# Performance work log

Hardware: AMD Instinct MI355X
Metric: run time of the kernel (lower is better)

The kernel has to match this reference:

```python
import jax, jax.numpy as jnp
import numpy as np

N = 50000      # nodes
E = 1_600_000  # edges (avg degree 32)
G = 2000       # graphs in batch
H = 2          # attention heads
C = 64         # out_channels
IN = 64        # in_channels
NEG_SLOPE = 0.2


def setup_inputs() -> dict:
    key = jax.random.key(0)
    ks = jax.random.split(key, 6)
    x = jax.random.normal(ks[0], (N, IN), dtype=jnp.float32)
    edge_index = jax.random.randint(ks[1], (2, E), 0, N, dtype=jnp.int32)
    batch = jnp.sort(jax.random.randint(ks[2], (N,), 0, G, dtype=jnp.int32))
    # GATConv params: lin weight [H*C, IN] (glorot-ish), att vectors, bias [C]
    W = jax.random.normal(ks[3], (H * C, IN), dtype=jnp.float32) * (1.0 / np.sqrt(IN))
    att_src = jax.random.normal(ks[4], (1, H, C), dtype=jnp.float32) * 0.1
    att_dst = jax.random.normal(ks[5], (1, H, C), dtype=jnp.float32) * 0.1
    bias = jnp.zeros((C,), dtype=jnp.float32)
    return {"x": x, "edge_index": edge_index, "batch": batch,
            "W": W, "att_src": att_src, "att_dst": att_dst, "bias": bias}


def reference(x, edge_index, batch, W, att_src, att_dst, bias):
    # --- GATConv (PyG semantics: add_self_loops=True, concat=False -> head mean + bias) ---
    loops = jnp.arange(N, dtype=edge_index.dtype)
    src = jnp.concatenate([edge_index[0], loops])  # [E+N]
    dst = jnp.concatenate([edge_index[1], loops])  # [E+N]

    xp = (x @ W.T).reshape(N, H, C)                 # projected node feats [N,H,C]
    a_src = jnp.sum(xp * att_src, axis=-1)          # [N,H]
    a_dst = jnp.sum(xp * att_dst, axis=-1)          # [N,H]

    e = jax.nn.leaky_relu(a_src[src] + a_dst[dst], NEG_SLOPE)  # [E+N,H]
    # segment softmax over incoming edges of each destination node
    m = jax.ops.segment_max(e, dst, num_segments=N)            # [N,H]
    e = jnp.exp(e - m[dst])
    s = jax.ops.segment_sum(e, dst, num_segments=N)            # [N,H]
    alpha = e / s[dst]                                         # [E+N,H]

    msg = xp[src] * alpha[:, :, None]                          # [E+N,H,C]
    out = jax.ops.segment_sum(msg, dst, num_segments=N)        # [N,H,C]
    h_nodes = out.mean(axis=1) + bias                          # [N,C]

    # --- global_mean_pool ---
    sums = jax.ops.segment_sum(h_nodes, batch, num_segments=G)                     # [G,C]
    cnt = jax.ops.segment_sum(jnp.ones((N, 1), h_nodes.dtype), batch, num_segments=G)
    h_graphs = sums / jnp.maximum(cnt, 1.0)                                        # [G,C]
    return (h_nodes, h_graphs)
```

## Files before the change

### kernel.cpp

```cpp
#include <hip/hip_runtime.h>
#include <hip/hip_bf16.h>

#define H 2
#define C 64
#define IN_CH 64
#define HC (H*C)
#define NEG_SLOPE 0.2f
#define NBUCK_MAX 256
#define NBLK 1024

__global__ __launch_bounds__(128) void proj_kernel(
    const float* __restrict__ x, const float* __restrict__ W,
    const float* __restrict__ att_src, const float* __restrict__ att_dst,
    __hip_bfloat16* __restrict__ xp, float* __restrict__ asrc,
    float* __restrict__ adst, int N) {
    int t = threadIdx.x;
    float w[64];
    const float4* wr = reinterpret_cast<const float4*>(W + (size_t)t * IN_CH);
#pragma unroll
    for (int q = 0; q < 16; q++) {
        float4 v = wr[q];
        w[4 * q] = v.x; w[4 * q + 1] = v.y; w[4 * q + 2] = v.z; w[4 * q + 3] = v.w;
    }
    float a_s = att_src[t], a_d = att_dst[t];
    int lane = t & 63, head = t >> 6;
    for (int n = blockIdx.x; n < N; n += gridDim.x) {
        const float* xr = x + (size_t)n * IN_CH;
        float acc = 0.f;
#pragma unroll
        for (int k = 0; k < 64; k++) acc = fmaf(w[k], xr[k], acc);
        xp[(size_t)n * HC + t] = __float2bfloat16(acc);
        float as = acc * a_s, ad = acc * a_d;
#pragma unroll
        for (int d = 32; d > 0; d >>= 1) {
            as += __shfl_xor(as, d, 64);
            ad += __shfl_xor(ad, d, 64);
        }
        if (lane == 0) {
            asrc[(size_t)n * H + head] = as;
            adst[(size_t)n * H + head] = ad;
        }
    }
}

__global__ __launch_bounds__(256) void hist_kernel(const int* __restrict__ dstE,
                                                   int* __restrict__ hist,
                                                   int E, int nbuck, int chunkE) {
    __shared__ int lh[NBUCK_MAX];
    for (int t = threadIdx.x; t < nbuck; t += 256) lh[t] = 0;
    __syncthreads();
    int beg = blockIdx.x * chunkE;
    int end = min(beg + chunkE, E);
    for (int i = beg + threadIdx.x; i < end; i += 256)
        atomicAdd(&lh[dstE[i] >> 8], 1);
    __syncthreads();
    for (int t = threadIdx.x; t < nbuck; t += 256)
        hist[t * NBLK + blockIdx.x] = lh[t];
}

__global__ __launch_bounds__(256) void scan_rows_kernel(int* __restrict__ hist,
                                                        int* __restrict__ rowsum) {
    int b = blockIdx.x, t = threadIdx.x;
    int* row = hist + b * NBLK;
    int v[4];
    int s = 0;
#pragma unroll
    for (int j = 0; j < 4; j++) { v[j] = row[t * 4 + j]; s += v[j]; }
    __shared__ int sh[256];
    sh[t] = s;
    __syncthreads();
    for (int d = 1; d < 256; d <<= 1) {
        int u = (t >= d) ? sh[t - d] : 0;
        __syncthreads();
        sh[t] += u;
        __syncthreads();
    }
    int run = sh[t] - s;
#pragma unroll
    for (int j = 0; j < 4; j++) { row[t * 4 + j] = run; run += v[j]; }
    if (t == 255) rowsum[b] = sh[255];
}

__global__ __launch_bounds__(256) void scan_base_kernel(int* __restrict__ rowsum,
                                                        int* __restrict__ bucketBase,
                                                        int nbuck) {
    int t = threadIdx.x;
    int v = (t < nbuck) ? rowsum[t] : 0;
    __shared__ int sh[256];
    sh[t] = v;
    __syncthreads();
    for (int d = 1; d < 256; d <<= 1) {
        int u = (t >= d) ? sh[t - d] : 0;
        __syncthreads();
        sh[t] += u;
        __syncthreads();
    }
    if (t < nbuck) bucketBase[t] = sh[t] - v;
    if (t == nbuck - 1) bucketBase[nbuck] = sh[t];
}

__global__ __launch_bounds__(256) void bucket_scatter_kernel(
    const int* __restrict__ srcE, const int* __restrict__ dstE,
    const int* __restrict__ hist, const int* __restrict__ bucketBase,
    int* __restrict__ staged, int E, int nbuck, int chunkE) {
    __shared__ int cur[NBUCK_MAX];
    for (int t = threadIdx.x; t < nbuck; t += 256)
        cur[t] = hist[t * NBLK + blockIdx.x] + bucketBase[t];
    __syncthreads();
    int beg = blockIdx.x * chunkE;
    int end = min(beg + chunkE, E);
    for (int i = beg + threadIdx.x; i < end; i += 256) {
        int s = srcE[i], d = dstE[i];
        int pos = atomicAdd(&cur[d >> 8], 1);
        staged[pos] = s | ((d & 255) << 20);
    }
}

__global__ __launch_bounds__(512) void bucket_csr_kernel(
    const int* __restrict__ staged, const int* __restrict__ bucketBase,
    int* __restrict__ off, int* __restrict__ csr, int N) {
    int b = blockIdx.x, t = threadIdx.x;
    int beg = bucketBase[b], end = bucketBase[b + 1];
    __shared__ int lh[256], sh[256], cur[256];
    if (t < 256) lh[t] = 0;
    __syncthreads();
    for (int i = beg + t; i < end; i += 512)
        atomicAdd(&lh[staged[i] >> 20], 1);
    __syncthreads();
    int v = (t < 256) ? lh[t] : 0;
    if (t < 256) sh[t] = v;
    __syncthreads();
    for (int d = 1; d < 256; d <<= 1) {
        int u = (t >= d && t < 256) ? sh[t - d] : 0;
        __syncthreads();
        if (t < 256) sh[t] += u;
        __syncthreads();
    }
    if (t < 256) {
        int ex = sh[t] - v;
        int nd = b * 256 + t;
        if (nd < N) off[nd] = beg + ex;
        if (nd == N - 1) off[N] = end;
        cur[t] = beg + ex;
    }
    __syncthreads();
    for (int i = beg + t; i < end; i += 512) {
        int e = staged[i];
        int pos = atomicAdd(&cur[e >> 20], 1);
        csr[pos] = e & 0xFFFFF;
    }
}

__global__ __launch_bounds__(256) void aggregate_kernel(
    const __hip_bfloat16* __restrict__ xp, const float2* __restrict__ asrc,
    const float2* __restrict__ adst, const int* __restrict__ off,
    const int* __restrict__ csr, const float* __restrict__ bias,
    const int* __restrict__ batch, float* __restrict__ out,
    float* __restrict__ gsum, int* __restrict__ gcnt, int N) {
    __shared__ float4 stage[4][64];
    int wid = threadIdx.x >> 6;
    int n = blockIdx.x * 4 + wid;
    if (n >= N) return;
    int lane = threadIdx.x & 63;
    float4* st = stage[wid];
    int o0 = off[n];
    int degE = off[n + 1] - o0;
    float2 ad = adst[n];
    float2 asn = asrc[n];
    float es0 = asn.x + ad.x; es0 = (es0 > 0.f) ? es0 : NEG_SLOPE * es0;
    float es1 = asn.y + ad.y; es1 = (es1 > 0.f) ? es1 : NEG_SLOPE * es1;
    float ws0 = __expf(es0), ws1 = __expf(es1);
    float s0 = (lane == 0) ? ws0 : 0.f;
    float s1 = (lane == 0) ? ws1 : 0.f;

    const uint* xpw = reinterpret_cast<const uint*>(xp);
    float accx, accy;
    {
        float wgt = (lane < 32) ? ws0 : ws1;
        uint u = xpw[(size_t)n * 64 + lane];
        accx = wgt * __uint_as_float(u << 16);
        accy = wgt * __uint_as_float(u & 0xffff0000u);
    }

    for (int base = 0; base < degE; base += 64) {
        int i = base + lane;
        int idx = 0;
        float w0 = 0.f, w1 = 0.f;
        if (i < degE) {
            idx = csr[o0 + i];
            float2 as = asrc[idx];
            float t0 = as.x + ad.x; t0 = (t0 > 0.f) ? t0 : NEG_SLOPE * t0;
            float t1 = as.y + ad.y; t1 = (t1 > 0.f) ? t1 : NEG_SLOPE * t1;
            w0 = __expf(t0);
            w1 = __expf(t1);
        }
        s0 += w0;
        s1 += w1;
        st[lane] = make_float4(__int_as_float(idx), w0, w1, 0.f);
        int cnt = min(degE - base, 64);
        int nb16 = (cnt + 15) >> 4;
        for (int b = 0; b < nb16; b++) {
            float4 e[16];
#pragma unroll
            for (int j = 0; j < 16; j++) e[j] = st[b * 16 + j];
            uint bu[16];
#pragma unroll
            for (int j = 0; j < 16; j++) {
                int s2 = __float_as_int(e[j].x);
                bu[j] = xpw[(size_t)s2 * 64 + lane];
            }
#pragma unroll
            for (int j = 0; j < 16; j++) {
                float wgt = (lane < 32) ? e[j].y : e[j].z;
                accx = fmaf(wgt, __uint_as_float(bu[j] << 16), accx);
                accy = fmaf(wgt, __uint_as_float(bu[j] & 0xffff0000u), accy);
            }
        }
    }
#pragma unroll
    for (int d = 32; d > 0; d >>= 1) {
        s0 += __shfl_xor(s0, d, 64);
        s1 += __shfl_xor(s1, d, 64);
    }
    float inv = (lane < 32) ? (1.f / s0) : (1.f / s1);
    accx *= inv;
    accy *= inv;
    float ox = 0.5f * (accx + __shfl_xor(accx, 32, 64));
    float oy = 0.5f * (accy + __shfl_xor(accy, 32, 64));
    int g = batch[n];
    if (lane < 32) {
        float vx = ox + bias[2 * lane];
        float vy = oy + bias[2 * lane + 1];
        *reinterpret_cast<float2*>(out + (size_t)n * C + 2 * lane) = make_float2(vx, vy);
        atomicAdd(&gsum[(size_t)g * C + 2 * lane], vx);
        atomicAdd(&gsum[(size_t)g * C + 2 * lane + 1], vy);
    }
    if (lane == 0) atomicAdd(&gcnt[g], 1);
}

__global__ void pool_kernel(const float* __restrict__ gsum, const int* __restrict__ gcnt,
                            float* __restrict__ out, int G, int baseOff) {
    int i = blockIdx.x * blockDim.x + threadIdx.x;
    if (i >= G * C) return;
    int g = i >> 6;
    float cnt = (float)max(gcnt[g], 1);
    out[baseOff + i] = gsum[i] / cnt;
}

extern "C" void kernel_launch(void* const* d_in, const int* in_sizes, int n_in,
                              void* d_out, int out_size, void* d_ws, size_t ws_size,
                              hipStream_t stream) {
    const float* x       = (const float*)d_in[0];
    const int*   edge    = (const int*)d_in[1];
    const int*   batch   = (const int*)d_in[2];
    const float* W       = (const float*)d_in[3];
    const float* att_src = (const float*)d_in[4];
    const float* att_dst = (const float*)d_in[5];
    const float* bias    = (const float*)d_in[6];

    int N = in_sizes[0] / IN_CH;
    int E = in_sizes[1] / 2;
    int G = out_size / C - N;
    int nbuck = (N + 255) >> 8;
    int chunkE = (E + NBLK - 1) / NBLK;

    char* p = (char*)d_ws;
    auto alloc = [&](size_t bytes) {
        char* r = p;
        p += (bytes + 255) & ~(size_t)255;
        return r;
    };
    __hip_bfloat16* xp = (__hip_bfloat16*)alloc((size_t)N * HC * 2);
    float* asrc    = (float*)alloc((size_t)N * H * 4);
    float* adst    = (float*)alloc((size_t)N * H * 4);
    int*   hist    = (int*)alloc((size_t)nbuck * NBLK * 4);
    int*   rowsum  = (int*)alloc((size_t)(nbuck + 1) * 4);
    int*   bucketBase = (int*)alloc((size_t)(nbuck + 1) * 4);
    int*   off     = (int*)alloc((size_t)(N + 1) * 4);
    int*   staged  = (int*)alloc((size_t)E * 4);
    int*   csr     = (int*)alloc((size_t)E * 4);
    float* gsum    = (float*)alloc((size_t)G * C * 4);
    int*   gcnt    = (int*)alloc((size_t)G * 4);

    hipMemsetAsync(gsum, 0, (size_t)G * C * 4, stream);
    hipMemsetAsync(gcnt, 0, (size_t)G * 4, stream);

    const int* srcE = edge;
    const int* dstE = edge + E;

    proj_kernel<<<2048, 128, 0, stream>>>(x, W, att_src, att_dst, xp, asrc, adst, N);
    hist_kernel<<<NBLK, 256, 0, stream>>>(dstE, hist, E, nbuck, chunkE);
    scan_rows_kernel<<<nbuck, 256, 0, stream>>>(hist, rowsum);
    scan_base_kernel<<<1, 256, 0, stream>>>(rowsum, bucketBase, nbuck);
    bucket_scatter_kernel<<<NBLK, 256, 0, stream>>>(srcE, dstE, hist, bucketBase,
                                                    staged, E, nbuck, chunkE);
    bucket_csr_kernel<<<nbuck, 512, 0, stream>>>(staged, bucketBase, off, csr, N);
    aggregate_kernel<<<(N + 3) / 4, 256, 0, stream>>>(xp, (const float2*)asrc, (const float2*)adst,
                                                      off, csr, bias, batch,
                                                      (float*)d_out, gsum, gcnt, N);
    pool_kernel<<<(G * C + 255) / 256, 256, 0, stream>>>(gsum, gcnt, (float*)d_out, G, N * C);
}
```

Measured before the change: 235.7 us.

## Fuse base scan into scatter/CSR kernels, split LDS staging, replace atomic pooling

```diff
diff --git a/kernel.cpp b/kernel.cpp
--- a/kernel.cpp
+++ b/kernel.cpp
@@ -81,35 +81,34 @@
     if (t == 255) rowsum[b] = sh[255];
 }
 
-__global__ __launch_bounds__(256) void scan_base_kernel(int* __restrict__ rowsum,
-                                                        int* __restrict__ bucketBase,
-                                                        int nbuck) {
-    int t = threadIdx.x;
+__device__ __forceinline__ void base_scan(const int* rowsum, int nbuck,
+                                          int* bse, int* rs, int t) {
     int v = (t < nbuck) ? rowsum[t] : 0;
-    __shared__ int sh[256];
-    sh[t] = v;
+    if (t < 256) { bse[t] = v; rs[t] = v; }
     __syncthreads();
     for (int d = 1; d < 256; d <<= 1) {
-        int u = (t >= d) ? sh[t - d] : 0;
-        __syncthreads();
-        sh[t] += u;
-        __syncthreads();
-    }
-    if (t < nbuck) bucketBase[t] = sh[t] - v;
-    if (t == nbuck - 1) bucketBase[nbuck] = sh[t];
+        int u = (t >= d && t < 256) ? bse[t - d] : 0;
+        __syncthreads();
+        if (t < 256) bse[t] += u;
+        __syncthreads();
+    }
+    if (t < 256) bse[t] -= rs[t];
+    __syncthreads();
 }
 
 __global__ __launch_bounds__(256) void bucket_scatter_kernel(
     const int* __restrict__ srcE, const int* __restrict__ dstE,
-    const int* __restrict__ hist, const int* __restrict__ bucketBase,
+    const int* __restrict__ hist, const int* __restrict__ rowsum,
     int* __restrict__ staged, int E, int nbuck, int chunkE) {
-    __shared__ int cur[NBUCK_MAX];
-    for (int t = threadIdx.x; t < nbuck; t += 256)
-        cur[t] = hist[t * NBLK + blockIdx.x] + bucketBase[t];
+    __shared__ int bse[256], rs[256], cur[NBUCK_MAX];
+    int t = threadIdx.x;
+    base_scan(rowsum, nbuck, bse, rs, t);
+    for (int i = t; i < nbuck; i += 256)
+        cur[i] = hist[i * NBLK + blockIdx.x] + bse[i];
     __syncthreads();
     int beg = blockIdx.x * chunkE;
     int end = min(beg + chunkE, E);
-    for (int i = beg + threadIdx.x; i < end; i += 256) {
+    for (int i = beg + t; i < end; i += 256) {
         int s = srcE[i], d = dstE[i];
         int pos = atomicAdd(&cur[d >> 8], 1);
         staged[pos] = s | ((d & 255) << 20);
@@ -117,11 +116,12 @@
 }
 
 __global__ __launch_bounds__(512) void bucket_csr_kernel(
-    const int* __restrict__ staged, const int* __restrict__ bucketBase,
-    int* __restrict__ off, int* __restrict__ csr, int N) {
+    const int* __restrict__ staged, const int* __restrict__ rowsum,
+    int* __restrict__ off, int* __restrict__ csr, int N, int nbuck, int E) {
     int b = blockIdx.x, t = threadIdx.x;
-    int beg = bucketBase[b], end = bucketBase[b + 1];
-    __shared__ int lh[256], sh[256], cur[256];
+    __shared__ int bse[256], rs[256], lh[256], sh[256], cur[256];
+    base_scan(rowsum, nbuck, bse, rs, t);
+    int beg = bse[b], end = beg + rs[b];
     if (t < 256) lh[t] = 0;
     __syncthreads();
     for (int i = beg + t; i < end; i += 512)
@@ -151,18 +151,39 @@
     }
 }
 
-__global__ __launch_bounds__(256) void aggregate_kernel(
+template<int NB16>
+__device__ __forceinline__ void gather_fma(const uint* __restrict__ xpw,
+                                           const int* __restrict__ sidx,
+                                           const float2* __restrict__ swt,
+                                           int lane, float& accx, float& accy) {
+    uint bu[NB16 * 16];
+#pragma unroll
+    for (int j = 0; j < NB16 * 16; j++) {
+        int s2 = sidx[j];
+        bu[j] = xpw[(size_t)s2 * 64 + lane];
+    }
+#pragma unroll
+    for (int j = 0; j < NB16 * 16; j++) {
+        float2 wv = swt[j];
+        float wgt = (lane < 32) ? wv.x : wv.y;
+        accx = fmaf(wgt, __uint_as_float(bu[j] << 16), accx);
+        accy = fmaf(wgt, __uint_as_float(bu[j] & 0xffff0000u), accy);
+    }
+}
+
+__global__ __launch_bounds__(256, 4) void aggregate_kernel(
     const __hip_bfloat16* __restrict__ xp, const float2* __restrict__ asrc,
     const float2* __restrict__ adst, const int* __restrict__ off,
     const int* __restrict__ csr, const float* __restrict__ bias,
-    const int* __restrict__ batch, float* __restrict__ out,
-    float* __restrict__ gsum, int* __restrict__ gcnt, int N) {
-    __shared__ float4 stage[4][64];
+    float* __restrict__ out, int N) {
+    __shared__ int sidx[4][64];
+    __shared__ float2 swt[4][64];
     int wid = threadIdx.x >> 6;
     int n = blockIdx.x * 4 + wid;
     if (n >= N) return;
     int lane = threadIdx.x & 63;
-    float4* st = stage[wid];
+    int* si = sidx[wid];
+    float2* sw = swt[wid];
     int o0 = off[n];
     int degE = off[n + 1] - o0;
     float2 ad = adst[n];
@@ -196,25 +217,15 @@
         }
         s0 += w0;
         s1 += w1;
-        st[lane] = make_float4(__int_as_float(idx), w0, w1, 0.f);
+        si[lane] = idx;
+        sw[lane] = make_float2(w0, w1);
         int cnt = min(degE - base, 64);
         int nb16 = (cnt + 15) >> 4;
-        for (int b = 0; b < nb16; b++) {
-            float4 e[16];
-#pragma unroll
-            for (int j = 0; j < 16; j++) e[j] = st[b * 16 + j];
-            uint bu[16];
-#pragma unroll
-            for (int j = 0; j < 16; j++) {
-                int s2 = __float_as_int(e[j].x);
-                bu[j] = xpw[(size_t)s2 * 64 + lane];
-            }
-#pragma unroll
-            for (int j = 0; j < 16; j++) {
-                float wgt = (lane < 32) ? e[j].y : e[j].z;
-                accx = fmaf(wgt, __uint_as_float(bu[j] << 16), accx);
-                accy = fmaf(wgt, __uint_as_float(bu[j] & 0xffff0000u), accy);
-            }
+        switch (nb16) {
+            case 1: gather_fma<1>(xpw, si, sw, lane, accx, accy); break;
+            case 2: gather_fma<2>(xpw, si, sw, lane, accx, accy); break;
+            case 3: gather_fma<3>(xpw, si, sw, lane, accx, accy); break;
+            default: gather_fma<4>(xpw, si, sw, lane, accx, accy); break;
         }
     }
 #pragma unroll
@@ -227,24 +238,27 @@
     accy *= inv;
     float ox = 0.5f * (accx + __shfl_xor(accx, 32, 64));
     float oy = 0.5f * (accy + __shfl_xor(accy, 32, 64));
-    int g = batch[n];
     if (lane < 32) {
         float vx = ox + bias[2 * lane];
         float vy = oy + bias[2 * lane + 1];
         *reinterpret_cast<float2*>(out + (size_t)n * C + 2 * lane) = make_float2(vx, vy);
-        atomicAdd(&gsum[(size_t)g * C + 2 * lane], vx);
-        atomicAdd(&gsum[(size_t)g * C + 2 * lane + 1], vy);
-    }
-    if (lane == 0) atomicAdd(&gcnt[g], 1);
-}
-
-__global__ void pool_kernel(const float* __restrict__ gsum, const int* __restrict__ gcnt,
-                            float* __restrict__ out, int G, int baseOff) {
-    int i = blockIdx.x * blockDim.x + threadIdx.x;
-    if (i >= G * C) return;
-    int g = i >> 6;
-    float cnt = (float)max(gcnt[g], 1);
-    out[baseOff + i] = gsum[i] / cnt;
+    }
+}
+
+__global__ __launch_bounds__(64) void pool_kernel(const float* __restrict__ hn,
+                                                  const int* __restrict__ batch,
+                                                  float* __restrict__ outG, int N, int G) {
+    int g = blockIdx.x;
+    int c = threadIdx.x;
+    int lo = 0, hi = N;
+    while (lo < hi) { int mid = (lo + hi) >> 1; if (batch[mid] < g) lo = mid + 1; else hi = mid; }
+    int beg = lo;
+    lo = beg; hi = N;
+    while (lo < hi) { int mid = (lo + hi) >> 1; if (batch[mid] < g + 1) lo = mid + 1; else hi = mid; }
+    int end = lo;
+    float s = 0.f;
+    for (int n = beg; n < end; n++) s += hn[(size_t)n * C + c];
+    outG[(size_t)g * C + c] = s / fmaxf((float)(end - beg), 1.f);
 }
 
 extern "C" void kernel_launch(void* const* d_in, const int* in_sizes, int n_in,
@@ -275,15 +289,9 @@
     float* adst    = (float*)alloc((size_t)N * H * 4);
     int*   hist    = (int*)alloc((size_t)nbuck * NBLK * 4);
     int*   rowsum  = (int*)alloc((size_t)(nbuck + 1) * 4);
-    int*   bucketBase = (int*)alloc((size_t)(nbuck + 1) * 4);
     int*   off     = (int*)alloc((size_t)(N + 1) * 4);
     int*   staged  = (int*)alloc((size_t)E * 4);
     int*   csr     = (int*)alloc((size_t)E * 4);
-    float* gsum    = (float*)alloc((size_t)G * C * 4);
-    int*   gcnt    = (int*)alloc((size_t)G * 4);
-
-    hipMemsetAsync(gsum, 0, (size_t)G * C * 4, stream);
-    hipMemsetAsync(gcnt, 0, (size_t)G * 4, stream);
 
     const int* srcE = edge;
     const int* dstE = edge + E;
@@ -291,12 +299,11 @@
     proj_kernel<<<2048, 128, 0, stream>>>(x, W, att_src, att_dst, xp, asrc, adst, N);
     hist_kernel<<<NBLK, 256, 0, stream>>>(dstE, hist, E, nbuck, chunkE);
     scan_rows_kernel<<<nbuck, 256, 0, stream>>>(hist, rowsum);
-    scan_base_kernel<<<1, 256, 0, stream>>>(rowsum, bucketBase, nbuck);
-    bucket_scatter_kernel<<<NBLK, 256, 0, stream>>>(srcE, dstE, hist, bucketBase,
+    bucket_scatter_kernel<<<NBLK, 256, 0, stream>>>(srcE, dstE, hist, rowsum,
                                                     staged, E, nbuck, chunkE);
-    bucket_csr_kernel<<<nbuck, 512, 0, stream>>>(staged, bucketBase, off, csr, N);
+    bucket_csr_kernel<<<nbuck, 512, 0, stream>>>(staged, rowsum, off, csr, N, nbuck, E);
     aggregate_kernel<<<(N + 3) / 4, 256, 0, stream>>>(xp, (const float2*)asrc, (const float2*)adst,
-                                                      off, csr, bias, batch,
-                                                      (float*)d_out, gsum, gcnt, N);
-    pool_kernel<<<(G * C + 255) / 256, 256, 0, stream>>>(gsum, gcnt, (float*)d_out, G, N * C);
-}
+                                                      off, csr, bias, (float*)d_out, N);
+    pool_kernel<<<G, 64, 0, stream>>>((const float*)d_out, batch, (float*)d_out + (size_t)N * C,
+                                      N, G);
+}
```

Measured after the change: 226.5 us. 3.9% less time.
